# Performance work log

Measured on AMD Instinct MI355X. Metric: run time of the kernel, lower is better.

## Reference

```python
import jax, jax.numpy as jnp
import numpy as np

HEAD_NUM = 16
NEG_BIG = -2.0**32 + 1.0


def _pos_encoding(T, D):
    pos = np.arange(T)[:, None].astype(np.float64)
    i = np.arange(D)[None, :].astype(np.float64)
    angle = pos / np.power(10000.0, 2.0 * i / D)
    pe = np.empty((T, D), dtype=np.float64)
    pe[:, 0::2] = np.sin(angle[:, 0::2])
    pe[:, 1::2] = np.cos(angle[:, 1::2])
    return jnp.asarray(pe * (D ** 0.5), dtype=jnp.float32)  # scale=True


def setup_inputs() -> dict:
    key = jax.random.key(0)
    ks = jax.random.split(key, 9)
    B, T, D = 32, 512, 1024
    return {
        "queries": jax.random.normal(ks[0], (B, T, D), jnp.float32),
        "keys": jax.random.normal(ks[1], (B, T, D), jnp.float32),
        "query_masks": jax.random.randint(ks[2], (B, 1), 1, T + 1, jnp.int32),
        "key_masks": jax.random.randint(ks[3], (B, 1), 1, T + 1, jnp.int32),
        "W_Query": jax.random.normal(ks[4], (D, D), jnp.float32) * 0.02,
        "W_key": jax.random.normal(ks[5], (D, D), jnp.float32) * 0.02,
        "W_Value": jax.random.normal(ks[6], (D, D), jnp.float32) * 0.02,
        "fw1": jax.random.normal(ks[7], (D, 4 * D), jnp.float32) * 0.02,
        "fw2": jax.random.normal(ks[8], (4 * D, D), jnp.float32) * 0.02,
    }


def reference(queries, keys, query_masks, key_masks, W_Query, W_key, W_Value, fw1, fw2):
    B, T, D = queries.shape
    h = HEAD_NUM
    d = D // h
    pe = _pos_encoding(T, D)  # [T, D]

    # faithful to source: queries get PE; keys = PE(queries_with_PE) (keys input unused)
    q_pe = queries + pe[None]
    k_pe = q_pe + pe[None]

    qs = jnp.einsum('btd,de->bte', q_pe, W_Query)
    ks_ = jnp.einsum('btd,de->bte', k_pe, W_key)
    vs = jnp.einsum('btd,de->bte', ks_, W_Value)  # faithful: values from projected keys

    def split_heads(x):  # [B,T,h*d] -> [h,B,T,d] (matches tf.split/concat on axis 0)
        return x.reshape(B, T, h, d).transpose(2, 0, 1, 3)

    q4, k4, v4 = split_heads(qs), split_heads(ks_), split_heads(vs)

    scores = jnp.einsum('hbqd,hbkd->hbqk', q4, k4) / (d ** 0.5)

    pos = jnp.arange(T)
    km = (pos[None, :] < key_masks).astype(jnp.float32)    # [B,T]
    qm = (pos[None, :] < query_masks).astype(jnp.float32)  # [B,T]

    scores = jnp.where(km[None, :, None, :] == 1.0, scores, NEG_BIG)
    scores = scores - jnp.max(scores, axis=-1, keepdims=True)
    attn = jax.nn.softmax(scores, axis=-1)
    attn = attn * qm[None, :, :, None]

    out = jnp.einsum('hbqk,hbkd->hbqd', attn, v4)
    result = out.transpose(1, 2, 0, 3).reshape(B, T, D)  # merge heads (head-major)

    result = result + q_pe  # use_res
    # feed forward (use_layer_norm=False, no dropout at inference)
    hmid = jax.nn.relu(jnp.einsum('btd,df->btf', result, fw1))
    result = result + jnp.einsum('btf,fd->btd', hmid, fw2)

    # output_type == 'mean'
    return jnp.mean(result, axis=1, keepdims=True)  # [B,1,D]
```

## Files before the change

kernel.cpp:

```cpp
#include <hip/hip_runtime.h>

constexpr int B_  = 32;
constexpr int T_  = 512;
constexpr int D_  = 1024;
constexpr int NH_ = 16;
constexpr int DH_ = 64;
constexpr int F_  = 4096;
constexpr int BT_ = B_ * T_;

typedef __attribute__((ext_vector_type(8))) short bf16x8;
typedef __attribute__((ext_vector_type(4))) float f32x4;

#define DEVI __device__ __forceinline__

DEVI unsigned short f2bf(float f) {
  union { float f; unsigned u; } uf; uf.f = f;
  unsigned r = uf.u + 0x7fffu + ((uf.u >> 16) & 1u);
  return (unsigned short)(r >> 16);
}
DEVI float b2f(unsigned short h) {
  union { unsigned u; float f; } uf; uf.u = ((unsigned)h) << 16;
  return uf.f;
}
DEVI void gload16(const void* g, void* l) {
  __builtin_amdgcn_global_load_lds(
      (const __attribute__((address_space(1))) void*)(uintptr_t)g,
      (__attribute__((address_space(3))) void*)(unsigned)(uintptr_t)l, 16, 0, 0);
}

__global__ void pe_kernel(float* __restrict__ pe) {
  int idx = blockIdx.x * 256 + threadIdx.x;
  int t = idx >> 10, j = idx & 1023;
  float inv = exp2f(-(2.0f * (float)j / 1024.0f) * 13.2877123795494f);
  float ang = (float)t * inv;
  float v = (j & 1) ? cosf(ang) : sinf(ang);
  pe[idx] = v * 32.0f;
}

__global__ void pack_kernel(const float* __restrict__ q, const float* __restrict__ pe,
                            unsigned short* __restrict__ q_pe, unsigned short* __restrict__ k_pe) {
  long i = ((long)blockIdx.x * 256 + threadIdx.x) * 4;
  const float4 qv = *(const float4*)(q + i);
  const float4 pv = *(const float4*)(pe + (i & (long)(T_ * D_ - 1)));
  ushort4 a, b;
  a.x = f2bf(qv.x + pv.x); a.y = f2bf(qv.y + pv.y);
  a.z = f2bf(qv.z + pv.z); a.w = f2bf(qv.w + pv.w);
  b.x = f2bf(qv.x + 2.f * pv.x); b.y = f2bf(qv.y + 2.f * pv.y);
  b.z = f2bf(qv.z + 2.f * pv.z); b.w = f2bf(qv.w + 2.f * pv.w);
  *(ushort4*)(q_pe + i) = a;
  *(ushort4*)(k_pe + i) = b;
}

__global__ void transpose_w(const float* __restrict__ W, unsigned short* __restrict__ Wt,
                            int K, int N) {
  __shared__ float tile[32][33];
  int tx = threadIdx.x & 31, ty = threadIdx.x >> 5;
  int bx = blockIdx.x, by = blockIdx.y;
  for (int i = 0; i < 4; i++) {
    int r = by * 32 + ty + i * 8;
    tile[ty + i * 8][tx] = W[(long)r * N + bx * 32 + tx];
  }
  __syncthreads();
  for (int i = 0; i < 4; i++) {
    int r = bx * 32 + ty + i * 8;
    Wt[(long)r * K + by * 32 + tx] = f2bf(tile[tx][ty + i * 8]);
  }
}

__global__ void cast_bf16(const float* __restrict__ W, unsigned short* __restrict__ Wb) {
  long i = ((long)blockIdx.x * 256 + threadIdx.x) * 4;
  const float4 v = *(const float4*)(W + i);
  ushort4 o;
  o.x = f2bf(v.x); o.y = f2bf(v.y); o.z = f2bf(v.z); o.w = f2bf(v.w);
  *(ushort4*)(Wb + i) = o;
}

__global__ void transpose_v(const unsigned short* __restrict__ vs, unsigned short* __restrict__ vt) {
  __shared__ unsigned short tile[64][65];
  int bh = blockIdx.y;
  int t0 = blockIdx.x * 64;
  int b = bh >> 4, h = bh & 15;
  int tx = threadIdx.x & 63, ty = threadIdx.x >> 6;
  for (int i = 0; i < 16; i++) {
    int r = i * 4 + ty;
    tile[r][tx] = vs[(long)(b * T_ + t0 + r) * D_ + h * DH_ + tx];
  }
  __syncthreads();
  for (int i = 0; i < 16; i++) {
    int j = i * 4 + ty;
    vt[((long)bh * DH_ + j) * T_ + t0 + tx] = tile[tx][j];
  }
}

template <int EPI>
__global__ __launch_bounds__(256) void gemm_bt(
    const unsigned short* __restrict__ A0, const unsigned short* __restrict__ Bt0,
    unsigned short* __restrict__ C0, float* __restrict__ hacc, int M, int N, int K) {
  __shared__ unsigned short As[128 * 32];
  __shared__ unsigned short Bs[128 * 32];
  const unsigned short* A  = A0;
  const unsigned short* Bt = Bt0;
  unsigned short* C        = C0;

  const int tid = threadIdx.x;
  const int lane = tid & 63, w = tid >> 6;
  const int wr = w >> 1, wc = w & 1;
  const int l15 = lane & 15, lhi = lane >> 4;
  const int brow = blockIdx.y * 128, bcol = blockIdx.x * 128;

  f32x4 acc[4][4] = {};
  const int o = tid * 16;
  const int srow = o >> 6;
  const int skel = (o & 63) >> 1;

  for (int kk = 0; kk < K; kk += 32) {
    gload16(A + (long)(brow + srow) * K + kk + skel,        (char*)As + o);
    gload16(A + (long)(brow + srow + 64) * K + kk + skel,   (char*)As + o + 4096);
    gload16(Bt + (long)(bcol + srow) * K + kk + skel,       (char*)Bs + o);
    gload16(Bt + (long)(bcol + srow + 64) * K + kk + skel,  (char*)Bs + o + 4096);
    __syncthreads();
    bf16x8 af[4], bfr[4];
    for (int m = 0; m < 4; m++)
      af[m] = *(const bf16x8*)((const char*)As + ((wr * 64 + m * 16 + l15) * 64 + lhi * 16));
    for (int n = 0; n < 4; n++)
      bfr[n] = *(const bf16x8*)((const char*)Bs + ((wc * 64 + n * 16 + l15) * 64 + lhi * 16));
    for (int m = 0; m < 4; m++)
      for (int n = 0; n < 4; n++)
        acc[m][n] = __builtin_amdgcn_mfma_f32_16x16x32_bf16(af[m], bfr[n], acc[m][n], 0, 0, 0);
    __syncthreads();
  }

  for (int m = 0; m < 4; m++)
    for (int n = 0; n < 4; n++) {
      int row = brow + wr * 64 + m * 16 + lhi * 4;
      int col = bcol + wc * 64 + n * 16 + l15;
      for (int r = 0; r < 4; r++)
        C[(long)(row + r) * N + col] = f2bf(acc[m][n][r]);
    }
}

template <int EPI>
__global__ __launch_bounds__(512, 2) void gemm8(
    const unsigned short* __restrict__ A0, const unsigned short* __restrict__ Bt0, unsigned short* __restrict__ C0,
    const unsigned short* __restrict__ A1, const unsigned short* __restrict__ Bt1, unsigned short* __restrict__ C1,
    const unsigned short* __restrict__ A2, const unsigned short* __restrict__ Bt2, unsigned short* __restrict__ C2,
    float* __restrict__ hacc, int N) {
  constexpr int K = 1024, NK = 16, NI = 8;
  __shared__ char lds[2][2][32768];

  const int z = blockIdx.z;
  const unsigned short* A  = (z == 0) ? A0  : (z == 1 ? A1  : A2);
  const unsigned short* Bt = (z == 0) ? Bt0 : (z == 1 ? Bt1 : Bt2);
  unsigned short* C        = (z == 0) ? C0  : (z == 1 ? C1  : C2);

  const int tid = threadIdx.x;
  const int lane = tid & 63, w = tid >> 6;
  const int wm = w >> 2, wn = w & 3;
  const int l15 = lane & 15, lhi = lane >> 4;
  const long brow = (long)blockIdx.x * 256, bcol = (long)blockIdx.y * 256;

  const int drow = (tid * 16) >> 7;
  const int dcol = ((tid * 16) & 127) ^ ((drow & 7) << 4);
  const int sw   = (l15 & 7) << 4;

  f32x4 acc[8][4] = {};
  bf16x8 bfr[4][2], af[2][2];

  auto STAGE = [&](const unsigned short* __restrict__ P, long tb, int kt, int h, int buf, int op) {
    const unsigned short* g = P + (tb + h * 128 + drow) * (long)K + kt * 64 + (dcol >> 1);
    char* l = &lds[buf][op][h * 16384 + tid * 16];
    gload16(g, l);
    gload16(g + 64L * K, l + 8192);
  };
  auto LDA = [&](int buf, int q) {
#pragma unroll
    for (int mi = 0; mi < 2; mi++) {
      int row = wm * 128 + (q * 2 + mi) * 16 + l15;
#pragma unroll
      for (int kk = 0; kk < 2; kk++)
        af[mi][kk] = *(const bf16x8*)(&lds[buf][0][0] + (row << 7) + ((kk * 64 + lhi * 16) ^ sw));
    }
  };
  auto LDB = [&](int buf) {
#pragma unroll
    for (int n = 0; n < 4; n++) {
      int row = wn * 64 + n * 16 + l15;
#pragma unroll
      for (int kk = 0; kk < 2; kk++)
        bfr[n][kk] = *(const bf16x8*)(&lds[buf][1][0] + (row << 7) + ((kk * 64 + lhi * 16) ^ sw));
    }
  };
  auto MFMAQ = [&](int q) {
    __builtin_amdgcn_s_setprio(1);
#pragma unroll
    for (int mi = 0; mi < 2; mi++)
#pragma unroll
      for (int n = 0; n < 4; n++)
#pragma unroll
        for (int kk = 0; kk < 2; kk++)
          acc[q * 2 + mi][n] =
              __builtin_amdgcn_mfma_f32_16x16x32_bf16(af[mi][kk], bfr[n][kk], acc[q * 2 + mi][n], 0, 0, 0);
    __builtin_amdgcn_s_setprio(0);
  };
#define BAR() __builtin_amdgcn_s_barrier()
#define GATE4() asm volatile("s_waitcnt vmcnt(4)" ::: "memory")

  STAGE(A, brow, 0, 0, 0, 0);  STAGE(A, brow, 0, 1, 0, 0);
  STAGE(Bt, bcol, 0, 0, 0, 1); STAGE(Bt, bcol, 0, 1, 0, 1);
  STAGE(Bt, bcol, 1, 0, 1, 1); STAGE(Bt, bcol, 1, 1, 1, 1);
  GATE4();
  BAR();

  for (int i = 0; i < NI; ++i) {
    const int k1 = 2 * i + 1;
    const int ka = (2 * i + 2) & (NK - 1);
    const int kb = (2 * i + 3) & (NK - 1);
    LDA(0, 0); LDB(0); STAGE(A, brow, k1, 0, 1, 0);
    BAR(); MFMAQ(0); BAR();
    LDA(0, 1);         STAGE(A, brow, k1, 1, 1, 0);
    BAR(); MFMAQ(1); BAR();
    LDA(0, 2);         STAGE(Bt, bcol, ka, 0, 0, 1);
    BAR(); MFMAQ(2); BAR();
    LDA(0, 3);         STAGE(Bt, bcol, ka, 1, 0, 1);
    BAR(); MFMAQ(3);
    GATE4();
    BAR();
    LDA(1, 0); LDB(1); STAGE(A, brow, ka, 0, 0, 0);
    BAR(); MFMAQ(0); BAR();
    LDA(1, 1);         STAGE(A, brow, ka, 1, 0, 0);
    BAR(); MFMAQ(1); BAR();
    LDA(1, 2);         STAGE(Bt, bcol, kb, 0, 1, 1);
    BAR(); MFMAQ(2); BAR();
    LDA(1, 3);         STAGE(Bt, bcol, kb, 1, 1, 1);
    BAR(); MFMAQ(3);
    GATE4();
    BAR();
  }
#undef BAR
#undef GATE4

  if (EPI == 0) {
#pragma unroll
    for (int m = 0; m < 8; m++)
#pragma unroll
      for (int n = 0; n < 4; n++) {
        long row = brow + wm * 128 + m * 16 + lhi * 4;
        long col = bcol + wn * 64 + n * 16 + l15;
#pragma unroll
        for (int r = 0; r < 4; r++)
          C[(row + r) * (long)N + col] = f2bf(acc[m][n][r]);
      }
  } else {
    const int batch = (int)(brow >> 9);
#pragma unroll
    for (int n = 0; n < 4; n++) {
      float t = 0.f;
#pragma unroll
      for (int m = 0; m < 8; m++)
#pragma unroll
        for (int r = 0; r < 4; r++) t += fmaxf(acc[m][n][r], 0.f);
      t += __shfl_xor(t, 16);
      t += __shfl_xor(t, 32);
      if (lane < 16)
        atomicAdd(hacc + (long)batch * F_ + bcol + wn * 64 + n * 16 + l15, t);
    }
  }
}

__global__ __launch_bounds__(256, 3) void attn_kernel(
    const unsigned short* __restrict__ qs, const unsigned short* __restrict__ ks,
    const unsigned short* __restrict__ vt, const unsigned short* __restrict__ q_pe,
    const int* __restrict__ qmask, const int* __restrict__ kmask,
    unsigned short* __restrict__ res) {
  __shared__ unsigned short Ks[2][64 * 64];
  __shared__ unsigned short Vs[2][64 * 64];
  __shared__ unsigned short Ps[4][32 * 64];

  const int tid = threadIdx.x, lane = tid & 63, w = tid >> 6;
  const int l15 = lane & 15, lhi = lane >> 4;
  const int h = blockIdx.x, b = blockIdx.y, q0 = blockIdx.z * 128;
  const int qlen = qmask[b], kvlen = kmask[b];

  if (q0 >= qlen) {
    for (int e = tid; e < 128 * 64; e += 256) {
      int r = e >> 6, cc = e & 63;
      long addr = (long)(b * T_ + q0 + r) * D_ + h * DH_ + cc;
      res[addr] = q_pe[addr];
    }
    return;
  }

  bf16x8 qf[2][2];
  for (int m = 0; m < 2; m++)
    for (int k2 = 0; k2 < 2; k2++) {
      int t = q0 + w * 32 + m * 16 + l15;
      qf[m][k2] = *(const bf16x8*)(qs + (long)(b * T_ + t) * D_ + h * DH_ + k2 * 32 + lhi * 8);
    }

  f32x4 o[2][4] = {};
  float mrun[2][4], lrun[2][4];
  for (int m = 0; m < 2; m++)
    for (int r = 0; r < 4; r++) { mrun[m][r] = -3e38f; lrun[m][r] = 0.f; }

  const float SCL = 0.125f * 1.4426950408889634f;
  const int nc = (kvlen + 63) >> 6;

  auto stage = [&](int c, int buf) {
#pragma unroll
    for (int cl = 0; cl < 2; cl++) {
      int ob = cl * 4096 + tid * 16;
      int os = ob ^ (((ob >> 7) & 7) << 4);
      int r0 = os >> 7, cb = os & 127;
      gload16(ks + (long)(b * T_ + c * 64 + r0) * D_ + h * DH_ + (cb >> 1),
              (char*)&Ks[buf][0] + ob);
      gload16(vt + ((long)(b * NH_ + h) * DH_ + r0) * T_ + c * 64 + (cb >> 1),
              (char*)&Vs[buf][0] + ob);
    }
  };

  stage(0, 0);
  int cur = 0;
  for (int c = 0; c < nc; c++) {
    const int nxt = (c + 1 < nc) ? c + 1 : c;
    stage(nxt, cur ^ 1);
    asm volatile("s_waitcnt vmcnt(4)" ::: "memory");
    __builtin_amdgcn_sched_barrier(0);
    __builtin_amdgcn_s_barrier();

    f32x4 s[2][4] = {};
    for (int k2 = 0; k2 < 2; k2++)
      for (int n = 0; n < 4; n++) {
        int key = n * 16 + l15;
        int Ab = key * 128 + (k2 * 32 + lhi * 8) * 2;
        bf16x8 kf = *(const bf16x8*)((const char*)&Ks[cur][0] + (Ab ^ ((key & 7) << 4)));
        s[0][n] = __builtin_amdgcn_mfma_f32_16x16x32_bf16(qf[0][k2], kf, s[0][n], 0, 0, 0);
        s[1][n] = __builtin_amdgcn_mfma_f32_16x16x32_bf16(qf[1][k2], kf, s[1][n], 0, 0, 0);
      }

    if (c == nc - 1) {
      for (int n = 0; n < 4; n++)
        if (c * 64 + n * 16 + l15 >= kvlen)
          for (int m = 0; m < 2; m++) s[m][n] = f32x4{-3e38f, -3e38f, -3e38f, -3e38f};
    }

    for (int m = 0; m < 2; m++) {
      float mx[4];
      for (int r = 0; r < 4; r++) {
        float v = s[m][0][r];
        for (int n = 1; n < 4; n++) v = fmaxf(v, s[m][n][r]);
        mx[r] = v;
      }
      for (int msk = 1; msk < 16; msk <<= 1)
        for (int r = 0; r < 4; r++) mx[r] = fmaxf(mx[r], __shfl_xor(mx[r], msk));
      float corr[4];
      for (int r = 0; r < 4; r++) {
        float mn = fmaxf(mrun[m][r], mx[r]);
        corr[r] = exp2f((mrun[m][r] - mn) * SCL);
        mrun[m][r] = mn;
      }
      for (int nd = 0; nd < 4; nd++)
        for (int r = 0; r < 4; r++) o[m][nd][r] *= corr[r];
      float ps[4] = {0.f, 0.f, 0.f, 0.f};
      for (int n = 0; n < 4; n++)
        for (int r = 0; r < 4; r++) {
          float pval = exp2f((s[m][n][r] - mrun[m][r]) * SCL);
          s[m][n][r] = pval;
          ps[r] += pval;
        }
      for (int msk = 1; msk < 16; msk <<= 1)
        for (int r = 0; r < 4; r++) ps[r] += __shfl_xor(ps[r], msk);
      for (int r = 0; r < 4; r++) lrun[m][r] = lrun[m][r] * corr[r] + ps[r];
      for (int n = 0; n < 4; n++)
        for (int r = 0; r < 4; r++) {
          int row = m * 16 + lhi * 4 + r;
          int Ab = row * 128 + (n * 16 + l15) * 2;
          *(unsigned short*)((char*)&Ps[w][0] + (Ab ^ ((row & 7) << 4))) = f2bf(s[m][n][r]);
        }
    }
    asm volatile("" ::: "memory");

    for (int k4 = 0; k4 < 2; k4++) {
      bf16x8 pa[2];
      for (int m = 0; m < 2; m++) {
        int row = m * 16 + l15;
        int Ab = row * 128 + k4 * 64 + lhi * 16;
        pa[m] = *(const bf16x8*)((const char*)&Ps[w][0] + (Ab ^ ((row & 7) << 4)));
      }
      for (int nd = 0; nd < 4; nd++) {
        int dv = nd * 16 + l15;
        int Ab = dv * 128 + k4 * 64 + lhi * 16;
        bf16x8 vb = *(const bf16x8*)((const char*)&Vs[cur][0] + (Ab ^ ((dv & 7) << 4)));
        for (int m = 0; m < 2; m++)
          o[m][nd] = __builtin_amdgcn_mfma_f32_16x16x32_bf16(pa[m], vb, o[m][nd], 0, 0, 0);
      }
    }
    __builtin_amdgcn_s_barrier();
    cur ^= 1;
  }

  for (int m = 0; m < 2; m++)
    for (int r = 0; r < 4; r++) {
      int t = q0 + w * 32 + m * 16 + lhi * 4 + r;
      float inv = 1.0f / lrun[m][r];
      bool valid = t < qlen;
      for (int nd = 0; nd < 4; nd++) {
        long addr = (long)(b * T_ + t) * D_ + h * DH_ + nd * 16 + l15;
        float v = valid ? o[m][nd][r] * inv : 0.f;
        res[addr] = f2bf(v + b2f(q_pe[addr]));
      }
    }
}

__global__ void colmean_kernel(const unsigned short* __restrict__ res, float* __restrict__ racc) {
  int b = blockIdx.y, c = blockIdx.x * 256 + threadIdx.x;
  const unsigned short* p = res + (long)b * T_ * D_ + c;
  float s = 0.f;
  for (int t = 0; t < T_; t++) s += b2f(p[(long)t * D_]);
  racc[b * D_ + c] = s;
}

__global__ void initout_kernel(const float* __restrict__ racc, float* __restrict__ out) {
  int i = blockIdx.x * 256 + threadIdx.x;
  out[i] = racc[i] * (1.0f / 512.0f);
}

__global__ void final_kernel(const float* __restrict__ hacc, const float* __restrict__ fw2,
                             float* __restrict__ out) {
  int n = blockIdx.x * 64 + (threadIdx.x & 63);
  int bg = threadIdx.x >> 6;
  int f0 = blockIdx.y * 512;
  float acc[8] = {};
  for (int f = f0; f < f0 + 512; f++) {
    float wv = fw2[(long)f * D_ + n];
    for (int i = 0; i < 8; i++) acc[i] += hacc[(long)(bg * 8 + i) * F_ + f] * wv;
  }
  for (int i = 0; i < 8; i++)
    atomicAdd(out + (bg * 8 + i) * D_ + n, acc[i] * (1.0f / 512.0f));
}

extern "C" void kernel_launch(void* const* d_in, const int* in_sizes, int n_in,
                              void* d_out, int out_size, void* d_ws, size_t ws_size,
                              hipStream_t stream) {
  const float* queries = (const float*)d_in[0];
  const int*   qmask = (const int*)d_in[2];
  const int*   kmask = (const int*)d_in[3];
  const float* Wq  = (const float*)d_in[4];
  const float* Wk  = (const float*)d_in[5];
  const float* Wv  = (const float*)d_in[6];
  const float* fw1 = (const float*)d_in[7];
  const float* fw2 = (const float*)d_in[8];
  float* out = (float*)d_out;

  char* p = (char*)d_ws;
  auto alloc = [&](size_t bytes) -> char* {
    char* r = p; p += (bytes + 255) & ~(size_t)255; return r;
  };
  float*          pe   = (float*)alloc((size_t)T_ * D_ * 4);
  unsigned short* q_pe = (unsigned short*)alloc((size_t)BT_ * D_ * 2);
  unsigned short* k_pe = (unsigned short*)alloc((size_t)BT_ * D_ * 2);
  unsigned short* qs   = (unsigned short*)alloc((size_t)BT_ * D_ * 2);
  unsigned short* ksb  = (unsigned short*)alloc((size_t)BT_ * D_ * 2);
  unsigned short* vt   = (unsigned short*)alloc((size_t)BT_ * D_ * 2);
  unsigned short* res  = (unsigned short*)alloc((size_t)BT_ * D_ * 2);
  unsigned short* Wqt  = (unsigned short*)alloc((size_t)D_ * D_ * 2);
  unsigned short* Wkt  = (unsigned short*)alloc((size_t)D_ * D_ * 2);
  unsigned short* Wvt  = (unsigned short*)alloc((size_t)D_ * D_ * 2);
  unsigned short* Wkbf = (unsigned short*)alloc((size_t)D_ * D_ * 2);
  unsigned short* Wkvt = (unsigned short*)alloc((size_t)D_ * D_ * 2);
  unsigned short* fw1t = (unsigned short*)alloc((size_t)D_ * F_ * 2);
  float*          racc = (float*)alloc((size_t)B_ * D_ * 4);
  float*          hacc = (float*)alloc((size_t)B_ * F_ * 4);
  unsigned short* vs = res;

  hipMemsetAsync(hacc, 0, (size_t)B_ * F_ * 4, stream);

  pe_kernel<<<T_ * D_ / 256, 256, 0, stream>>>(pe);
  pack_kernel<<<BT_ * D_ / 1024, 256, 0, stream>>>(queries, pe, q_pe, k_pe);
  transpose_w<<<dim3(32, 32), 256, 0, stream>>>(Wq, Wqt, D_, D_);
  transpose_w<<<dim3(32, 32), 256, 0, stream>>>(Wk, Wkt, D_, D_);
  transpose_w<<<dim3(32, 32), 256, 0, stream>>>(Wv, Wvt, D_, D_);
  transpose_w<<<dim3(F_ / 32, 32), 256, 0, stream>>>(fw1, fw1t, D_, F_);
  cast_bf16<<<(D_ * D_) / 1024, 256, 0, stream>>>(Wk, Wkbf);

  gemm_bt<0><<<dim3(8, 8, 1), 256, 0, stream>>>(Wvt, Wkbf, Wkvt, nullptr, D_, D_, D_);

  gemm8<0><<<dim3(64, 4, 3), 512, 0, stream>>>(q_pe, Wqt, qs,
                                               k_pe, Wkt, ksb,
                                               k_pe, Wkvt, vs,
                                               nullptr, D_);

  transpose_v<<<dim3(8, 512), 256, 0, stream>>>(vs, vt);

  attn_kernel<<<dim3(16, 32, 4), 256, 0, stream>>>(qs, ksb, vt, q_pe, qmask, kmask, res);

  colmean_kernel<<<dim3(4, 32), 256, 0, stream>>>(res, racc);

  gemm8<1><<<dim3(64, 16, 1), 512, 0, stream>>>(res, fw1t, nullptr,
                                                res, fw1t, nullptr,
                                                res, fw1t, nullptr,
                                                hacc, F_);

  initout_kernel<<<(B_ * D_) / 256, 256, 0, stream>>>(racc, out);
  final_kernel<<<dim3(16, 8), 256, 0, stream>>>(hacc, fw2, out);
}
```

Baseline: 452.5 us.

## Use 32x32 MFMA tiles in gemm8 and skip fully-masked QKV row blocks

Switches the large GEMM from 16x16x32 to 32x32x16 bf16 MFMA instructions, restructuring the LDS fragment loads, accumulator layout and epilogues. The goal is fewer LDS reads per FLOP. It also passes the query/key length masks to the QKV projection so that 256-row blocks in the second half of a sequence exit early when the valid length is at most 256. Launch bounds drop to one block per CU to allow more registers. Skipped rows stay uninitialized, so downstream kernels must never consume them unmasked.

Result: slower. 468.3 us (+3.5%).

```diff
diff --git a/kernel.cpp b/kernel.cpp
--- a/kernel.cpp
+++ b/kernel.cpp
@@ -10,6 +10,7 @@
 
 typedef __attribute__((ext_vector_type(8))) short bf16x8;
 typedef __attribute__((ext_vector_type(4))) float f32x4;
+typedef __attribute__((ext_vector_type(16))) float f32x16;
 
 #define DEVI __device__ __forceinline__
 
@@ -140,11 +141,12 @@
 }
 
 template <int EPI>
-__global__ __launch_bounds__(512, 2) void gemm8(
+__global__ __launch_bounds__(512, 1) void gemm8(
     const unsigned short* __restrict__ A0, const unsigned short* __restrict__ Bt0, unsigned short* __restrict__ C0,
     const unsigned short* __restrict__ A1, const unsigned short* __restrict__ Bt1, unsigned short* __restrict__ C1,
     const unsigned short* __restrict__ A2, const unsigned short* __restrict__ Bt2, unsigned short* __restrict__ C2,
-    float* __restrict__ hacc, int N) {
+    float* __restrict__ hacc, int N,
+    const int* __restrict__ L0, const int* __restrict__ L1, const int* __restrict__ L2) {
   constexpr int K = 1024, NK = 16, NI = 8;
   __shared__ char lds[2][2][32768];
 
@@ -152,19 +154,20 @@
   const unsigned short* A  = (z == 0) ? A0  : (z == 1 ? A1  : A2);
   const unsigned short* Bt = (z == 0) ? Bt0 : (z == 1 ? Bt1 : Bt2);
   unsigned short* C        = (z == 0) ? C0  : (z == 1 ? C1  : C2);
+  const int* L             = (z == 0) ? L0  : (z == 1 ? L1  : L2);
+
+  const long brow = (long)blockIdx.x * 256, bcol = (long)blockIdx.y * 256;
+  if (L && (brow & 256) && L[brow >> 9] <= 256) return;
 
   const int tid = threadIdx.x;
   const int lane = tid & 63, w = tid >> 6;
   const int wm = w >> 2, wn = w & 3;
-  const int l15 = lane & 15, lhi = lane >> 4;
-  const long brow = (long)blockIdx.x * 256, bcol = (long)blockIdx.y * 256;
+  const int l31 = lane & 31, lh = lane >> 5;
 
   const int drow = (tid * 16) >> 7;
   const int dcol = ((tid * 16) & 127) ^ ((drow & 7) << 4);
-  const int sw   = (l15 & 7) << 4;
-
-  f32x4 acc[8][4] = {};
-  bf16x8 bfr[4][2], af[2][2];
+  f32x16 acc[4][2] = {};
+  bf16x8 af[4], bfr[2][4];
 
   auto STAGE = [&](const unsigned short* __restrict__ P, long tb, int kt, int h, int buf, int op) {
     const unsigned short* g = P + (tb + h * 128 + drow) * (long)K + kt * 64 + (dcol >> 1);
@@ -174,32 +177,27 @@
   };
   auto LDA = [&](int buf, int q) {
 #pragma unroll
-    for (int mi = 0; mi < 2; mi++) {
-      int row = wm * 128 + (q * 2 + mi) * 16 + l15;
-#pragma unroll
-      for (int kk = 0; kk < 2; kk++)
-        af[mi][kk] = *(const bf16x8*)(&lds[buf][0][0] + (row << 7) + ((kk * 64 + lhi * 16) ^ sw));
+    for (int mt = 0; mt < 4; mt++) {
+      int row = wm * 128 + mt * 32 + l31;
+      af[mt] = *(const bf16x8*)(&lds[buf][0][0] + (row << 7) + ((q * 32 + lh * 16) ^ ((row & 7) << 4)));
     }
   };
-  auto LDB = [&](int buf) {
-#pragma unroll
-    for (int n = 0; n < 4; n++) {
-      int row = wn * 64 + n * 16 + l15;
-#pragma unroll
-      for (int kk = 0; kk < 2; kk++)
-        bfr[n][kk] = *(const bf16x8*)(&lds[buf][1][0] + (row << 7) + ((kk * 64 + lhi * 16) ^ sw));
+  auto LDBALL = [&](int buf) {
+#pragma unroll
+    for (int nt = 0; nt < 2; nt++) {
+      int row = wn * 64 + nt * 32 + l31;
+#pragma unroll
+      for (int q = 0; q < 4; q++)
+        bfr[nt][q] = *(const bf16x8*)(&lds[buf][1][0] + (row << 7) + ((q * 32 + lh * 16) ^ ((row & 7) << 4)));
     }
   };
   auto MFMAQ = [&](int q) {
     __builtin_amdgcn_s_setprio(1);
 #pragma unroll
-    for (int mi = 0; mi < 2; mi++)
-#pragma unroll
-      for (int n = 0; n < 4; n++)
-#pragma unroll
-        for (int kk = 0; kk < 2; kk++)
-          acc[q * 2 + mi][n] =
-              __builtin_amdgcn_mfma_f32_16x16x32_bf16(af[mi][kk], bfr[n][kk], acc[q * 2 + mi][n], 0, 0, 0);
+    for (int mt = 0; mt < 4; mt++)
+#pragma unroll
+      for (int nt = 0; nt < 2; nt++)
+        acc[mt][nt] = __builtin_amdgcn_mfma_f32_32x32x16_bf16(af[mt], bfr[nt][q], acc[mt][nt], 0, 0, 0);
     __builtin_amdgcn_s_setprio(0);
   };
 #define BAR() __builtin_amdgcn_s_barrier()
@@ -215,23 +213,23 @@
     const int k1 = 2 * i + 1;
     const int ka = (2 * i + 2) & (NK - 1);
     const int kb = (2 * i + 3) & (NK - 1);
-    LDA(0, 0); LDB(0); STAGE(A, brow, k1, 0, 1, 0);
+    LDA(0, 0); LDBALL(0); STAGE(A, brow, k1, 0, 1, 0);
     BAR(); MFMAQ(0); BAR();
-    LDA(0, 1);         STAGE(A, brow, k1, 1, 1, 0);
+    LDA(0, 1);            STAGE(A, brow, k1, 1, 1, 0);
     BAR(); MFMAQ(1); BAR();
-    LDA(0, 2);         STAGE(Bt, bcol, ka, 0, 0, 1);
+    LDA(0, 2);            STAGE(Bt, bcol, ka, 0, 0, 1);
     BAR(); MFMAQ(2); BAR();
-    LDA(0, 3);         STAGE(Bt, bcol, ka, 1, 0, 1);
+    LDA(0, 3);            STAGE(Bt, bcol, ka, 1, 0, 1);
     BAR(); MFMAQ(3);
     GATE4();
     BAR();
-    LDA(1, 0); LDB(1); STAGE(A, brow, ka, 0, 0, 0);
+    LDA(1, 0); LDBALL(1); STAGE(A, brow, ka, 0, 0, 0);
     BAR(); MFMAQ(0); BAR();
-    LDA(1, 1);         STAGE(A, brow, ka, 1, 0, 0);
+    LDA(1, 1);            STAGE(A, brow, ka, 1, 0, 0);
     BAR(); MFMAQ(1); BAR();
-    LDA(1, 2);         STAGE(Bt, bcol, kb, 0, 1, 1);
+    LDA(1, 2);            STAGE(Bt, bcol, kb, 0, 1, 1);
     BAR(); MFMAQ(2); BAR();
-    LDA(1, 3);         STAGE(Bt, bcol, kb, 1, 1, 1);
+    LDA(1, 3);            STAGE(Bt, bcol, kb, 1, 1, 1);
     BAR(); MFMAQ(3);
     GATE4();
     BAR();
@@ -241,28 +239,28 @@
 
   if (EPI == 0) {
 #pragma unroll
-    for (int m = 0; m < 8; m++)
-#pragma unroll
-      for (int n = 0; n < 4; n++) {
-        long row = brow + wm * 128 + m * 16 + lhi * 4;
-        long col = bcol + wn * 64 + n * 16 + l15;
-#pragma unroll
-        for (int r = 0; r < 4; r++)
-          C[(row + r) * (long)N + col] = f2bf(acc[m][n][r]);
+    for (int mt = 0; mt < 4; mt++)
+#pragma unroll
+      for (int nt = 0; nt < 2; nt++) {
+        long col = bcol + wn * 64 + nt * 32 + l31;
+#pragma unroll
+        for (int reg = 0; reg < 16; reg++) {
+          long row = brow + wm * 128 + mt * 32 + (reg & 3) + 8 * (reg >> 2) + 4 * lh;
+          C[row * (long)N + col] = f2bf(acc[mt][nt][reg]);
+        }
       }
   } else {
     const int batch = (int)(brow >> 9);
 #pragma unroll
-    for (int n = 0; n < 4; n++) {
+    for (int nt = 0; nt < 2; nt++) {
       float t = 0.f;
 #pragma unroll
-      for (int m = 0; m < 8; m++)
-#pragma unroll
-        for (int r = 0; r < 4; r++) t += fmaxf(acc[m][n][r], 0.f);
-      t += __shfl_xor(t, 16);
+      for (int mt = 0; mt < 4; mt++)
+#pragma unroll
+        for (int reg = 0; reg < 16; reg++) t += fmaxf(acc[mt][nt][reg], 0.f);
       t += __shfl_xor(t, 32);
-      if (lane < 16)
-        atomicAdd(hacc + (long)batch * F_ + bcol + wn * 64 + n * 16 + l15, t);
+      if (lane < 32)
+        atomicAdd(hacc + (long)batch * F_ + bcol + wn * 64 + nt * 32 + l31, t);
     }
   }
 }
@@ -487,7 +485,7 @@
   gemm8<0><<<dim3(64, 4, 3), 512, 0, stream>>>(q_pe, Wqt, qs,
                                                k_pe, Wkt, ksb,
                                                k_pe, Wkvt, vs,
-                                               nullptr, D_);
+                                               nullptr, D_, qmask, kmask, kmask);
 
   transpose_v<<<dim3(8, 512), 256, 0, stream>>>(vs, vt);
 
@@ -498,7 +496,7 @@
   gemm8<1><<<dim3(64, 16, 1), 512, 0, stream>>>(res, fw1t, nullptr,
                                                 res, fw1t, nullptr,
                                                 res, fw1t, nullptr,
-                                                hacc, F_);
+                                                hacc, F_, nullptr, nullptr, nullptr);
 
   initout_kernel<<<(B_ * D_) / 256, 256, 0, stream>>>(racc, out);
   final_kernel<<<dim3(16, 8), 256, 0, stream>>>(hacc, fw2, out);
```

## Skip masked-out projection tiles and fuse column mean into attention epilogue

Applied to the files above, without the earlier changes.

The QKV projection GEMM now exits early for the second 256-row half of a batch when that batch's query or key mask length is at most 256. Those rows are either never read (keys and values beyond kvlen) or never needed (queries beyond qlen, whose results are overwritten with q_pe). The separate colmean kernel is removed; the attention kernel accumulates per-column sums in its epilogue and in the masked-copy path, then atomically adds them into racc, which is now zeroed first. This saves a full read of res and some GEMM work, at the cost of atomics and fp32 summation order differing from the old bf16 re-read.

Result: faster. 433.9 us (-4.1%).

```diff
diff --git a/kernel.cpp b/kernel.cpp
--- a/kernel.cpp
+++ b/kernel.cpp
@@ -144,7 +144,8 @@
     const unsigned short* __restrict__ A0, const unsigned short* __restrict__ Bt0, unsigned short* __restrict__ C0,
     const unsigned short* __restrict__ A1, const unsigned short* __restrict__ Bt1, unsigned short* __restrict__ C1,
     const unsigned short* __restrict__ A2, const unsigned short* __restrict__ Bt2, unsigned short* __restrict__ C2,
-    float* __restrict__ hacc, int N) {
+    float* __restrict__ hacc, int N,
+    const int* __restrict__ L0, const int* __restrict__ L1, const int* __restrict__ L2) {
   constexpr int K = 1024, NK = 16, NI = 8;
   __shared__ char lds[2][2][32768];
 
@@ -152,12 +153,15 @@
   const unsigned short* A  = (z == 0) ? A0  : (z == 1 ? A1  : A2);
   const unsigned short* Bt = (z == 0) ? Bt0 : (z == 1 ? Bt1 : Bt2);
   unsigned short* C        = (z == 0) ? C0  : (z == 1 ? C1  : C2);
+  const int* L             = (z == 0) ? L0  : (z == 1 ? L1  : L2);
+
+  const long brow = (long)blockIdx.x * 256, bcol = (long)blockIdx.y * 256;
+  if (L && (brow & 256) && L[brow >> 9] <= 256) return;
 
   const int tid = threadIdx.x;
   const int lane = tid & 63, w = tid >> 6;
   const int wm = w >> 2, wn = w & 3;
   const int l15 = lane & 15, lhi = lane >> 4;
-  const long brow = (long)blockIdx.x * 256, bcol = (long)blockIdx.y * 256;
 
   const int drow = (tid * 16) >> 7;
   const int dcol = ((tid * 16) & 127) ^ ((drow & 7) << 4);
@@ -271,7 +275,7 @@
     const unsigned short* __restrict__ qs, const unsigned short* __restrict__ ks,
     const unsigned short* __restrict__ vt, const unsigned short* __restrict__ q_pe,
     const int* __restrict__ qmask, const int* __restrict__ kmask,
-    unsigned short* __restrict__ res) {
+    unsigned short* __restrict__ res, float* __restrict__ racc) {
   __shared__ unsigned short Ks[2][64 * 64];
   __shared__ unsigned short Vs[2][64 * 64];
   __shared__ unsigned short Ps[4][32 * 64];
@@ -282,11 +286,16 @@
   const int qlen = qmask[b], kvlen = kmask[b];
 
   if (q0 >= qlen) {
-    for (int e = tid; e < 128 * 64; e += 256) {
-      int r = e >> 6, cc = e & 63;
+    int cc = tid & 63;
+    float s = 0.f;
+    for (int i = 0; i < 32; i++) {
+      int r = (tid >> 6) * 32 + i;
       long addr = (long)(b * T_ + q0 + r) * D_ + h * DH_ + cc;
-      res[addr] = q_pe[addr];
-    }
+      unsigned short v = q_pe[addr];
+      res[addr] = v;
+      s += b2f(v);
+    }
+    atomicAdd(racc + b * D_ + h * DH_ + cc, s);
     return;
   }
 
@@ -398,6 +407,7 @@
     cur ^= 1;
   }
 
+  float cs[4] = {0.f, 0.f, 0.f, 0.f};
   for (int m = 0; m < 2; m++)
     for (int r = 0; r < 4; r++) {
       int t = q0 + w * 32 + m * 16 + lhi * 4 + r;
@@ -406,17 +416,18 @@
       for (int nd = 0; nd < 4; nd++) {
         long addr = (long)(b * T_ + t) * D_ + h * DH_ + nd * 16 + l15;
         float v = valid ? o[m][nd][r] * inv : 0.f;
-        res[addr] = f2bf(v + b2f(q_pe[addr]));
-      }
-    }
-}
-
-__global__ void colmean_kernel(const unsigned short* __restrict__ res, float* __restrict__ racc) {
-  int b = blockIdx.y, c = blockIdx.x * 256 + threadIdx.x;
-  const unsigned short* p = res + (long)b * T_ * D_ + c;
-  float s = 0.f;
-  for (int t = 0; t < T_; t++) s += b2f(p[(long)t * D_]);
-  racc[b * D_ + c] = s;
+        float val = v + b2f(q_pe[addr]);
+        res[addr] = f2bf(val);
+        cs[nd] += val;
+      }
+    }
+  for (int nd = 0; nd < 4; nd++) {
+    cs[nd] += __shfl_xor(cs[nd], 16);
+    cs[nd] += __shfl_xor(cs[nd], 32);
+  }
+  if (lane < 16)
+    for (int nd = 0; nd < 4; nd++)
+      atomicAdd(racc + b * D_ + h * DH_ + nd * 16 + l15, cs[nd]);
 }
 
 __global__ void initout_kernel(const float* __restrict__ racc, float* __restrict__ out) {
@@ -473,6 +484,7 @@
   unsigned short* vs = res;
 
   hipMemsetAsync(hacc, 0, (size_t)B_ * F_ * 4, stream);
+  hipMemsetAsync(racc, 0, (size_t)B_ * D_ * 4, stream);
 
   pe_kernel<<<T_ * D_ / 256, 256, 0, stream>>>(pe);
   pack_kernel<<<BT_ * D_ / 1024, 256, 0, stream>>>(queries, pe, q_pe, k_pe);
@@ -487,18 +499,16 @@
   gemm8<0><<<dim3(64, 4, 3), 512, 0, stream>>>(q_pe, Wqt, qs,
                                                k_pe, Wkt, ksb,
                                                k_pe, Wkvt, vs,
-                                               nullptr, D_);
+                                               nullptr, D_, qmask, kmask, kmask);
 
   transpose_v<<<dim3(8, 512), 256, 0, stream>>>(vs, vt);
 
-  attn_kernel<<<dim3(16, 32, 4), 256, 0, stream>>>(qs, ksb, vt, q_pe, qmask, kmask, res);
-
-  colmean_kernel<<<dim3(4, 32), 256, 0, stream>>>(res, racc);
+  attn_kernel<<<dim3(16, 32, 4), 256, 0, stream>>>(qs, ksb, vt, q_pe, qmask, kmask, res, racc);
 
   gemm8<1><<<dim3(64, 16, 1), 512, 0, stream>>>(res, fw1t, nullptr,
                                                 res, fw1t, nullptr,
                                                 res, fw1t, nullptr,
-                                                hacc, F_);
+                                                hacc, F_, nullptr, nullptr, nullptr);
 
   initout_kernel<<<(B_ * D_) / 256, 256, 0, stream>>>(racc, out);
   final_kernel<<<dim3(16, 8), 256, 0, stream>>>(hacc, fw2, out);
```
